# Kernel optimization log

Hardware: AMD Instinct MI355X
Metric: run time of the kernel (lower is better)

## Reference

```python
import jax, jax.numpy as jnp
import numpy as np
import math

B, C, H, W = 16, 256, 128, 128
IC = 32  # inter_channels = in_channels // r


def setup_inputs() -> dict:
    key = jax.random.key(0)
    ks = jax.random.split(key, 7)
    s_in = 1.0 / math.sqrt(C)   # ~ conv kaiming-uniform scale for C->IC 1x1 conv
    s_out = 1.0 / math.sqrt(IC)  # for IC->C 1x1 conv
    return {
        "x": jax.random.normal(ks[0], (B, C, H, W), dtype=jnp.float32),
        "g_w": jax.random.normal(ks[1], (IC, C), dtype=jnp.float32) * s_in,
        "g_b": jax.random.normal(ks[2], (IC,), dtype=jnp.float32) * s_in,
        "theta_w": jax.random.normal(ks[3], (IC, C), dtype=jnp.float32) * s_in,
        "theta_b": jax.random.normal(ks[4], (IC,), dtype=jnp.float32) * s_in,
        "w_w": jax.random.normal(ks[5], (C, IC), dtype=jnp.float32) * s_out,
        "w_b": jax.random.normal(ks[6], (C,), dtype=jnp.float32) * s_out,
    }


def reference(x, g_w, g_b, theta_w, theta_b, w_w, w_b):
    b, c, h, w = x.shape
    m = h * w
    ic = g_w.shape[0]
    xf = x.reshape(b, c, m)  # (B, C, M)
    # 1x1 convs == per-pixel channel matmuls
    g_x = jnp.einsum('ic,bcm->bim', g_w, xf) + g_b[None, :, None]      # (B, IC, M)
    t = jnp.einsum('ic,bcm->bim', theta_w, xf) + theta_b[None, :, None]  # (B, IC, M)
    # sigma = theta_x_T @ I_hat @ theta_x with I_hat = I/M - 11^T/M^2
    #       = (t t^T)/M - mu mu^T  (closed form; avoids (M,M) matrix)
    mu = jnp.mean(t, axis=-1)  # (B, IC)
    sigma = jnp.einsum('bim,bjm->bij', t, t) / m - mu[:, :, None] * mu[:, None, :]
    sigma = sigma / math.sqrt(ic)
    attn = jax.nn.softmax(sigma, axis=-1)  # (B, IC, IC)
    y = jnp.einsum('bij,bjm->bim', attn, g_x)  # (B, IC, M)
    w_y = jnp.einsum('ci,bim->bcm', w_w, y) + w_b[None, :, None]  # (B, C, M)
    return (w_y + xf).reshape(b, c, h, w)
```

## Files before the change

### kernel.cpp

```cpp
#include <hip/hip_runtime.h>
#include <math.h>

constexpr int Bn  = 16;
constexpr int Cn  = 256;
constexpr int Mn  = 16384;
constexpr int ICn = 32;

typedef float v4f    __attribute__((ext_vector_type(4)));
typedef short short8 __attribute__((ext_vector_type(8)));

constexpr size_t OFF_WTH  = 0;
constexpr size_t OFF_TT   = OFF_WTH + 4096;
constexpr size_t OFF_MU   = OFF_TT  + (size_t)Bn * ICn * ICn;
constexpr size_t OFF_BEFF = OFF_MU  + (size_t)Bn * ICn;
constexpr size_t OFF_WIMG = OFF_BEFF + (size_t)Bn * Cn;

__device__ inline unsigned short f2bf(float f) {
    unsigned u = __float_as_uint(f);
    u += 0x7fffu + ((u >> 16) & 1u);
    return (unsigned short)(u >> 16);
}

__device__ inline void gload_lds16(const void* g, void* l) {
    __builtin_amdgcn_global_load_lds(
        (const __attribute__((address_space(1))) unsigned int*)g,
        (__attribute__((address_space(3))) unsigned int*)l,
        16, 0, 0);
}

__global__ void k0_prep_w(const float* __restrict__ th_w,
                          unsigned short* __restrict__ wbf) {
    int idx = blockIdx.x * 256 + threadIdx.x;
    int row = idx >> 8, ks = idx & 255;
    int slot = ks >> 3;
    int k = ((slot ^ (row & 7)) << 3) | (ks & 7);
    wbf[idx] = f2bf(th_w[row * Cn + k]);
}

__global__ __launch_bounds__(256, 4) void k1_stats(
    const float* __restrict__ x,
    const unsigned short* __restrict__ wbf,
    const float* __restrict__ theta_b,
    float* __restrict__ tt,
    float* __restrict__ mu)
{
    __shared__ __align__(16) unsigned short Ws[32 * 256];
    __shared__ __align__(16) unsigned short Ts[32 * 72];
    __shared__ float mu_s[ICn];

    const int tx   = threadIdx.x;
    const int b    = blockIdx.y;
    const int m0   = blockIdx.x * 64;
    const int lane = tx & 63;
    const int w    = tx >> 6;
    const int ln15 = lane & 15;
    const int q    = lane >> 4;

    {
        const int4* src = (const int4*)wbf;
        int4* dst = (int4*)Ws;
        #pragma unroll
        for (int i = 0; i < 4; ++i) dst[tx + 256 * i] = src[tx + 256 * i];
    }
    if (tx < ICn) mu_s[tx] = 0.f;
    __syncthreads();

    v4f acc[2];
    #pragma unroll
    for (int nt = 0; nt < 2; ++nt) acc[nt] = (v4f){0.f, 0.f, 0.f, 0.f};

    const float* xbase = x + ((size_t)b * Cn + q * 8) * Mn + m0 + w * 16 + ln15;

    float xf[8];
    #pragma unroll
    for (int j = 0; j < 8; ++j) xf[j] = xbase[(size_t)j * Mn];

    #pragma unroll
    for (int kc = 0; kc < 8; ++kc) {
        short8 a;
        #pragma unroll
        for (int j = 0; j < 8; ++j) a[j] = (short)f2bf(xf[j]);
        if (kc < 7) {
            #pragma unroll
            for (int j = 0; j < 8; ++j)
                xf[j] = xbase[(size_t)((kc + 1) * 32 + j) * Mn];
        }
        #pragma unroll
        for (int nt = 0; nt < 2; ++nt) {
            int row  = nt * 16 + ln15;
            int slot = (kc * 4 + q) ^ (row & 7);
            short8 bf = *(const short8*)&Ws[row * 256 + slot * 8];
            acc[nt] = __builtin_amdgcn_mfma_f32_16x16x32_bf16(a, bf, acc[nt], 0, 0, 0);
        }
    }

    #pragma unroll
    for (int nt = 0; nt < 2; ++nt) {
        int tr = nt * 16 + ln15;
        float bb = theta_b[tr];
        float s = 0.f;
        #pragma unroll
        for (int r = 0; r < 4; ++r) {
            float tv = acc[nt][r] + bb;
            Ts[tr * 72 + w * 16 + q * 4 + r] = f2bf(tv);
            s += tv;
        }
        s += __shfl_xor(s, 16);
        s += __shfl_xor(s, 32);
        if (q == 0) atomicAdd(&mu_s[tr], s);
    }
    __syncthreads();

    {
        int i0 = (w & 1) * 16, j0 = (w >> 1) * 16;
        v4f at = (v4f){0.f, 0.f, 0.f, 0.f};
        #pragma unroll
        for (int pc = 0; pc < 2; ++pc) {
            short8 A  = *(const short8*)&Ts[(i0 + ln15) * 72 + pc * 32 + q * 8];
            short8 Bv = *(const short8*)&Ts[(j0 + ln15) * 72 + pc * 32 + q * 8];
            at = __builtin_amdgcn_mfma_f32_16x16x32_bf16(A, Bv, at, 0, 0, 0);
        }
        float* ttb = tt + (size_t)b * ICn * ICn;
        #pragma unroll
        for (int r = 0; r < 4; ++r)
            atomicAdd(&ttb[(i0 + q * 4 + r) * ICn + j0 + ln15], at[r]);
    }
    if (tx < ICn) atomicAdd(&mu[b * ICn + tx], mu_s[tx]);
}

__global__ void k2_fold(const float* __restrict__ tt,
                        const float* __restrict__ mu_in,
                        const float* __restrict__ g_w,
                        const float* __restrict__ g_b,
                        const float* __restrict__ w_w,
                        const float* __restrict__ w_b,
                        unsigned short* __restrict__ wimg,
                        float* __restrict__ beff)
{
    __shared__ float s_mu[ICn];
    __shared__ float s_sig[ICn][ICn];
    __shared__ float s_attn[ICn][ICn + 1];
    __shared__ float s_gw[ICn][64];
    __shared__ float s_gb[ICn];

    const int b  = blockIdx.x;
    const int kc = blockIdx.y;
    const int tx = threadIdx.x;

    if (tx < ICn) s_mu[tx] = mu_in[b * ICn + tx] * (1.f / Mn);
    __syncthreads();

    for (int p = tx; p < ICn * ICn; p += 256) {
        int i = p >> 5, j = p & 31;
        s_sig[i][j] = (tt[b * ICn * ICn + p] * (1.f / Mn) - s_mu[i] * s_mu[j])
                      * 0.17677669529663687f;
    }
    for (int p = tx; p < ICn * 64; p += 256) {
        int j = p >> 6, kk = p & 63;
        s_gw[j][kk] = g_w[j * Cn + kc * 64 + kk];
    }
    if (tx < ICn) s_gb[tx] = g_b[tx];
    __syncthreads();

    if (tx < ICn) {
        float mx = -1e30f;
        #pragma unroll
        for (int j = 0; j < ICn; ++j) mx = fmaxf(mx, s_sig[tx][j]);
        float e[ICn];
        float sum = 0.f;
        #pragma unroll
        for (int j = 0; j < ICn; ++j) { e[j] = __expf(s_sig[tx][j] - mx); sum += e[j]; }
        float r = 1.f / sum;
        #pragma unroll
        for (int j = 0; j < ICn; ++j) s_attn[tx][j] = e[j] * r;
    }
    __syncthreads();

    const int c = tx;
    float wr[ICn];
    #pragma unroll
    for (int i = 0; i < ICn; i += 4) {
        float4 v = *(const float4*)(w_w + c * ICn + i);
        wr[i] = v.x; wr[i + 1] = v.y; wr[i + 2] = v.z; wr[i + 3] = v.w;
    }
    float a2[ICn];
    #pragma unroll
    for (int j = 0; j < ICn; ++j) {
        float s = 0.f;
        #pragma unroll
        for (int i = 0; i < ICn; ++i) s += wr[i] * s_attn[i][j];
        a2[j] = s;
    }
    unsigned short* wrow = wimg + ((size_t)b * Cn + c) * Cn;
    for (int kk = 0; kk < 64; ++kk) {
        int k = kc * 64 + kk;
        float v = 0.f;
        #pragma unroll
        for (int j = 0; j < ICn; ++j) v += a2[j] * s_gw[j][kk];
        int pos = (((k >> 3) ^ (c & 7)) << 3) | (k & 7);
        wrow[pos] = f2bf(v);
    }
    if (kc == 0) {
        float s = 0.f;
        #pragma unroll
        for (int i = 0; i < ICn; ++i) {
            float ab = 0.f;
            #pragma unroll
            for (int j = 0; j < ICn; ++j) ab += s_attn[i][j] * s_gb[j];
            s += wr[i] * ab;
        }
        beff[b * Cn + c] = s + w_b[c];
    }
}

__global__ __launch_bounds__(256, 2) void k3_out(
    const float* __restrict__ x,
    const unsigned short* __restrict__ wimg,
    const float* __restrict__ beff,
    float* __restrict__ out)
{
    __shared__ __align__(16) unsigned short Ws[128 * 256];
    __shared__ float bb[Cn];

    const int tx   = threadIdx.x;
    const int b    = blockIdx.y;
    const int m0   = blockIdx.x * 64;
    const int lane = tx & 63;
    const int w    = tx >> 6;
    const int ln15 = lane & 15;
    const int q    = lane >> 4;

    const char* gw0 = (const char*)(wimg + (size_t)b * Cn * Cn);

    #pragma unroll
    for (int i = 0; i < 16; ++i) {
        int seg = w * 16 + i;
        gload_lds16(gw0 + seg * 1024 + lane * 16, (char*)Ws + seg * 1024);
    }
    if (tx < 64) ((float4*)bb)[tx] = ((const float4*)(beff + b * Cn))[tx];

    const float* xbase = x + ((size_t)b * Cn + q * 8) * Mn + m0 + w * 16 + ln15;
    short8 a[8];
    #pragma unroll
    for (int kc = 0; kc < 8; ++kc) {
        float xf[8];
        #pragma unroll
        for (int j = 0; j < 8; ++j) xf[j] = xbase[(size_t)(kc * 32 + j) * Mn];
        #pragma unroll
        for (int j = 0; j < 8; ++j) a[kc][j] = (short)f2bf(xf[j]);
    }
    __syncthreads();

    const size_t obase = (size_t)b * Cn * Mn + m0 + w * 16 + q * 4;
    v4f acc[8];

    #pragma unroll
    for (int ct = 0; ct < 8; ++ct) acc[ct] = (v4f){0.f, 0.f, 0.f, 0.f};
    #pragma unroll
    for (int kc = 0; kc < 8; ++kc) {
        #pragma unroll
        for (int ct = 0; ct < 8; ++ct) {
            int row  = ct * 16 + ln15;
            int slot = (kc * 4 + q) ^ (row & 7);
            short8 bf = *(const short8*)&Ws[row * 256 + slot * 8];
            acc[ct] = __builtin_amdgcn_mfma_f32_16x16x32_bf16(a[kc], bf, acc[ct], 0, 0, 0);
        }
    }
    __syncthreads();

    #pragma unroll
    for (int i = 0; i < 16; ++i) {
        int seg = w * 16 + i;
        gload_lds16(gw0 + 65536 + seg * 1024 + lane * 16, (char*)Ws + seg * 1024);
    }
    #pragma unroll
    for (int ct = 0; ct < 8; ++ct) {
        int c = ct * 16 + ln15;
        float4 xv = *(const float4*)(x + obase + (size_t)c * Mn);
        float wb = bb[c];
        float4 o;
        o.x = acc[ct][0] + xv.x + wb;
        o.y = acc[ct][1] + xv.y + wb;
        o.z = acc[ct][2] + xv.z + wb;
        o.w = acc[ct][3] + xv.w + wb;
        *(float4*)(out + obase + (size_t)c * Mn) = o;
    }
    __syncthreads();

    #pragma unroll
    for (int ct = 0; ct < 8; ++ct) acc[ct] = (v4f){0.f, 0.f, 0.f, 0.f};
    #pragma unroll
    for (int kc = 0; kc < 8; ++kc) {
        #pragma unroll
        for (int ct = 0; ct < 8; ++ct) {
            int row  = ct * 16 + ln15;
            int slot = (kc * 4 + q) ^ (row & 7);
            short8 bf = *(const short8*)&Ws[row * 256 + slot * 8];
            acc[ct] = __builtin_amdgcn_mfma_f32_16x16x32_bf16(a[kc], bf, acc[ct], 0, 0, 0);
        }
    }
    #pragma unroll
    for (int ct = 0; ct < 8; ++ct) {
        int c = 128 + ct * 16 + ln15;
        float4 xv = *(const float4*)(x + obase + (size_t)c * Mn);
        float wb = bb[c];
        float4 o;
        o.x = acc[ct][0] + xv.x + wb;
        o.y = acc[ct][1] + xv.y + wb;
        o.z = acc[ct][2] + xv.z + wb;
        o.w = acc[ct][3] + xv.w + wb;
        *(float4*)(out + obase + (size_t)c * Mn) = o;
    }
}

extern "C" void kernel_launch(void* const* d_in, const int* in_sizes, int n_in,
                              void* d_out, int out_size, void* d_ws, size_t ws_size,
                              hipStream_t stream) {
    const float* x    = (const float*)d_in[0];
    const float* g_w  = (const float*)d_in[1];
    const float* g_b  = (const float*)d_in[2];
    const float* th_w = (const float*)d_in[3];
    const float* th_b = (const float*)d_in[4];
    const float* w_w  = (const float*)d_in[5];
    const float* w_b  = (const float*)d_in[6];
    float* out = (float*)d_out;
    float* ws  = (float*)d_ws;

    unsigned short* wth  = (unsigned short*)(ws + OFF_WTH);
    float* tt            = ws + OFF_TT;
    float* mu            = ws + OFF_MU;
    float* beff          = ws + OFF_BEFF;
    unsigned short* wimg = (unsigned short*)(ws + OFF_WIMG);

    hipMemsetAsync(tt, 0, (size_t)(Bn * ICn * ICn + Bn * ICn) * sizeof(float), stream);

    k0_prep_w<<<32, 256, 0, stream>>>(th_w, wth);
    k1_stats<<<dim3(Mn / 64, Bn), 256, 0, stream>>>(x, wth, th_b, tt, mu);
    k2_fold<<<dim3(Bn, 4), 256, 0, stream>>>(tt, mu, g_w, g_b, w_w, w_b, wimg, beff);
    k3_out<<<dim3(Mn / 64, Bn), 256, 0, stream>>>(x, wimg, beff, out);
}
```

Before: 623.5 us.

## Stage x through LDS with vectorized transposed loads; shrink k3 weight tile

Both k1_stats and k3_out now load x with coalesced float4 reads, convert to bf16 and write a transposed, XOR-swizzled tile into LDS. Each lane then reads its MFMA A-fragments from that tile, replacing the strided scalar per-channel global loads. k3_out reuses the same 32KB LDS buffer for 64-channel weight chunks in four passes, prefetching the residual x values one pass ahead. This lowers LDS use so occupancy can rise to 4 blocks, at the cost of more barriers and serialized weight reloads.

```diff
diff --git a/kernel.cpp b/kernel.cpp
--- a/kernel.cpp
+++ b/kernel.cpp
@@ -37,13 +37,37 @@
     wbf[idx] = f2bf(th_w[row * Cn + k]);
 }
 
-__global__ __launch_bounds__(256, 4) void k1_stats(
+__device__ inline void load_transpose_x(const float* __restrict__ xb,
+                                        unsigned short* Xs, int tx) {
+    #pragma unroll
+    for (int i = 0; i < 4; ++i) {
+        int c0  = i * 64 + (tx >> 4) * 4;
+        int px0 = (tx & 15) * 4;
+        v4f v[4];
+        #pragma unroll
+        for (int cc = 0; cc < 4; ++cc)
+            v[cc] = *(const v4f*)(xb + (size_t)(c0 + cc) * Mn + px0);
+        #pragma unroll
+        for (int r = 0; r < 4; ++r) {
+            int px = px0 + r;
+            unsigned long long pk =
+                  (unsigned long long)f2bf(v[0][r])
+                | ((unsigned long long)f2bf(v[1][r]) << 16)
+                | ((unsigned long long)f2bf(v[2][r]) << 32)
+                | ((unsigned long long)f2bf(v[3][r]) << 48);
+            *(unsigned long long*)((char*)Xs + px * 512 + ((c0 * 2) ^ ((px & 7) << 4))) = pk;
+        }
+    }
+}
+
+__global__ __launch_bounds__(256, 3) void k1_stats(
     const float* __restrict__ x,
     const unsigned short* __restrict__ wbf,
     const float* __restrict__ theta_b,
     float* __restrict__ tt,
     float* __restrict__ mu)
 {
+    __shared__ __align__(16) unsigned short Xs[64 * 256];
     __shared__ __align__(16) unsigned short Ws[32 * 256];
     __shared__ __align__(16) unsigned short Ts[32 * 72];
     __shared__ float mu_s[ICn];
@@ -56,52 +80,50 @@
     const int ln15 = lane & 15;
     const int q    = lane >> 4;
 
+    #pragma unroll
+    for (int i = 0; i < 4; ++i) {
+        int seg = w * 4 + i;
+        gload_lds16((const char*)wbf + seg * 1024 + lane * 16, (char*)Ws + seg * 1024);
+    }
+
+    const float* xb = x + (size_t)b * Cn * Mn + m0;
+    load_transpose_x(xb, Xs, tx);
+
+    if (tx < ICn) mu_s[tx] = 0.f;
+    __syncthreads();
+
+    short8 a[8];
     {
-        const int4* src = (const int4*)wbf;
-        int4* dst = (int4*)Ws;
-        #pragma unroll
-        for (int i = 0; i < 4; ++i) dst[tx + 256 * i] = src[tx + 256 * i];
-    }
-    if (tx < ICn) mu_s[tx] = 0.f;
-    __syncthreads();
+        int px = w * 16 + ln15;
+        #pragma unroll
+        for (int kc = 0; kc < 8; ++kc)
+            a[kc] = *(const short8*)((const char*)Xs + px * 512
+                                     + ((kc * 64 + q * 16) ^ ((px & 7) << 4)));
+    }
 
     v4f acc[2];
     #pragma unroll
     for (int nt = 0; nt < 2; ++nt) acc[nt] = (v4f){0.f, 0.f, 0.f, 0.f};
 
-    const float* xbase = x + ((size_t)b * Cn + q * 8) * Mn + m0 + w * 16 + ln15;
-
-    float xf[8];
-    #pragma unroll
-    for (int j = 0; j < 8; ++j) xf[j] = xbase[(size_t)j * Mn];
-
     #pragma unroll
     for (int kc = 0; kc < 8; ++kc) {
-        short8 a;
-        #pragma unroll
-        for (int j = 0; j < 8; ++j) a[j] = (short)f2bf(xf[j]);
-        if (kc < 7) {
-            #pragma unroll
-            for (int j = 0; j < 8; ++j)
-                xf[j] = xbase[(size_t)((kc + 1) * 32 + j) * Mn];
-        }
         #pragma unroll
         for (int nt = 0; nt < 2; ++nt) {
             int row  = nt * 16 + ln15;
             int slot = (kc * 4 + q) ^ (row & 7);
             short8 bf = *(const short8*)&Ws[row * 256 + slot * 8];
-            acc[nt] = __builtin_amdgcn_mfma_f32_16x16x32_bf16(a, bf, acc[nt], 0, 0, 0);
+            acc[nt] = __builtin_amdgcn_mfma_f32_16x16x32_bf16(a[kc], bf, acc[nt], 0, 0, 0);
         }
     }
 
     #pragma unroll
     for (int nt = 0; nt < 2; ++nt) {
         int tr = nt * 16 + ln15;
-        float bb = theta_b[tr];
+        float bbv = theta_b[tr];
         float s = 0.f;
         #pragma unroll
         for (int r = 0; r < 4; ++r) {
-            float tv = acc[nt][r] + bb;
+            float tv = acc[nt][r] + bbv;
             Ts[tr * 72 + w * 16 + q * 4 + r] = f2bf(tv);
             s += tv;
         }
@@ -213,13 +235,13 @@
     }
 }
 
-__global__ __launch_bounds__(256, 2) void k3_out(
+__global__ __launch_bounds__(256, 4) void k3_out(
     const float* __restrict__ x,
     const unsigned short* __restrict__ wimg,
     const float* __restrict__ beff,
     float* __restrict__ out)
 {
-    __shared__ __align__(16) unsigned short Ws[128 * 256];
+    __shared__ __align__(16) unsigned short Xs[64 * 256];
     __shared__ float bb[Cn];
 
     const int tx   = threadIdx.x;
@@ -230,86 +252,83 @@
     const int ln15 = lane & 15;
     const int q    = lane >> 4;
 
+    const float* xb = x + (size_t)b * Cn * Mn + m0;
+
+    load_transpose_x(xb, Xs, tx);
+    if (tx < 64) ((float4*)bb)[tx] = ((const float4*)(beff + b * Cn))[tx];
+
+    const size_t obase = (size_t)b * Cn * Mn + m0 + w * 16 + q * 4;
+    v4f xv[4];
+    #pragma unroll
+    for (int ct = 0; ct < 4; ++ct)
+        xv[ct] = *(const v4f*)(x + obase + (size_t)(ct * 16 + ln15) * Mn);
+
+    __syncthreads();
+
+    short8 a[8];
+    {
+        int px = w * 16 + ln15;
+        #pragma unroll
+        for (int kc = 0; kc < 8; ++kc)
+            a[kc] = *(const short8*)((const char*)Xs + px * 512
+                                     + ((kc * 64 + q * 16) ^ ((px & 7) << 4)));
+    }
+    __syncthreads();
+
     const char* gw0 = (const char*)(wimg + (size_t)b * Cn * Cn);
 
     #pragma unroll
-    for (int i = 0; i < 16; ++i) {
-        int seg = w * 16 + i;
-        gload_lds16(gw0 + seg * 1024 + lane * 16, (char*)Ws + seg * 1024);
-    }
-    if (tx < 64) ((float4*)bb)[tx] = ((const float4*)(beff + b * Cn))[tx];
-
-    const float* xbase = x + ((size_t)b * Cn + q * 8) * Mn + m0 + w * 16 + ln15;
-    short8 a[8];
-    #pragma unroll
-    for (int kc = 0; kc < 8; ++kc) {
-        float xf[8];
-        #pragma unroll
-        for (int j = 0; j < 8; ++j) xf[j] = xbase[(size_t)(kc * 32 + j) * Mn];
-        #pragma unroll
-        for (int j = 0; j < 8; ++j) a[kc][j] = (short)f2bf(xf[j]);
-    }
-    __syncthreads();
-
-    const size_t obase = (size_t)b * Cn * Mn + m0 + w * 16 + q * 4;
-    v4f acc[8];
-
-    #pragma unroll
-    for (int ct = 0; ct < 8; ++ct) acc[ct] = (v4f){0.f, 0.f, 0.f, 0.f};
-    #pragma unroll
-    for (int kc = 0; kc < 8; ++kc) {
-        #pragma unroll
-        for (int ct = 0; ct < 8; ++ct) {
-            int row  = ct * 16 + ln15;
-            int slot = (kc * 4 + q) ^ (row & 7);
-            short8 bf = *(const short8*)&Ws[row * 256 + slot * 8];
-            acc[ct] = __builtin_amdgcn_mfma_f32_16x16x32_bf16(a[kc], bf, acc[ct], 0, 0, 0);
-        }
-    }
-    __syncthreads();
-
-    #pragma unroll
-    for (int i = 0; i < 16; ++i) {
-        int seg = w * 16 + i;
-        gload_lds16(gw0 + 65536 + seg * 1024 + lane * 16, (char*)Ws + seg * 1024);
-    }
-    #pragma unroll
-    for (int ct = 0; ct < 8; ++ct) {
-        int c = ct * 16 + ln15;
-        float4 xv = *(const float4*)(x + obase + (size_t)c * Mn);
-        float wb = bb[c];
-        float4 o;
-        o.x = acc[ct][0] + xv.x + wb;
-        o.y = acc[ct][1] + xv.y + wb;
-        o.z = acc[ct][2] + xv.z + wb;
-        o.w = acc[ct][3] + xv.w + wb;
-        *(float4*)(out + obase + (size_t)c * Mn) = o;
-    }
-    __syncthreads();
-
-    #pragma unroll
-    for (int ct = 0; ct < 8; ++ct) acc[ct] = (v4f){0.f, 0.f, 0.f, 0.f};
-    #pragma unroll
-    for (int kc = 0; kc < 8; ++kc) {
-        #pragma unroll
-        for (int ct = 0; ct < 8; ++ct) {
-            int row  = ct * 16 + ln15;
-            int slot = (kc * 4 + q) ^ (row & 7);
-            short8 bf = *(const short8*)&Ws[row * 256 + slot * 8];
-            acc[ct] = __builtin_amdgcn_mfma_f32_16x16x32_bf16(a[kc], bf, acc[ct], 0, 0, 0);
-        }
-    }
-    #pragma unroll
-    for (int ct = 0; ct < 8; ++ct) {
-        int c = 128 + ct * 16 + ln15;
-        float4 xv = *(const float4*)(x + obase + (size_t)c * Mn);
-        float wb = bb[c];
-        float4 o;
-        o.x = acc[ct][0] + xv.x + wb;
-        o.y = acc[ct][1] + xv.y + wb;
-        o.z = acc[ct][2] + xv.z + wb;
-        o.w = acc[ct][3] + xv.w + wb;
-        *(float4*)(out + obase + (size_t)c * Mn) = o;
+    for (int i = 0; i < 8; ++i) {
+        int seg = w * 8 + i;
+        gload_lds16(gw0 + seg * 1024 + lane * 16, (char*)Xs + seg * 1024);
+    }
+    __syncthreads();
+
+    #pragma unroll
+    for (int n = 0; n < 4; ++n) {
+        v4f acc[4];
+        #pragma unroll
+        for (int ct = 0; ct < 4; ++ct) acc[ct] = (v4f){0.f, 0.f, 0.f, 0.f};
+        #pragma unroll
+        for (int kc = 0; kc < 8; ++kc) {
+            #pragma unroll
+            for (int ct = 0; ct < 4; ++ct) {
+                int row  = ct * 16 + ln15;
+                int slot = (kc * 4 + q) ^ (row & 7);
+                short8 bf = *(const short8*)&Xs[row * 256 + slot * 8];
+                acc[ct] = __builtin_amdgcn_mfma_f32_16x16x32_bf16(a[kc], bf, acc[ct], 0, 0, 0);
+            }
+        }
+        __syncthreads();
+
+        if (n < 3) {
+            #pragma unroll
+            for (int i = 0; i < 8; ++i) {
+                int seg = w * 8 + i;
+                gload_lds16(gw0 + (size_t)(n + 1) * 32768 + seg * 1024 + lane * 16,
+                            (char*)Xs + seg * 1024);
+            }
+        }
+
+        #pragma unroll
+        for (int ct = 0; ct < 4; ++ct) {
+            int c = n * 64 + ct * 16 + ln15;
+            float wb2 = bb[c];
+            v4f o;
+            o[0] = acc[ct][0] + xv[ct][0] + wb2;
+            o[1] = acc[ct][1] + xv[ct][1] + wb2;
+            o[2] = acc[ct][2] + xv[ct][2] + wb2;
+            o[3] = acc[ct][3] + xv[ct][3] + wb2;
+            *(v4f*)(out + obase + (size_t)c * Mn) = o;
+        }
+
+        if (n < 3) {
+            #pragma unroll
+            for (int ct = 0; ct < 4; ++ct)
+                xv[ct] = *(const v4f*)(x + obase
+                          + (size_t)((n + 1) * 64 + ct * 16 + ln15) * Mn);
+            __syncthreads();
+        }
     }
 }
 
```

New measurement: 610.4 us. 2.1% less time.
